# Performance work log

Measured on AMD Instinct MI355X. Metric: run time of the kernel, lower is better.

The kernel has to match this reference:

```python
import jax, jax.numpy as jnp
import numpy as np

N = 50000      # nodes
E = 625000     # edges
D_IN = 128     # in_feats
D_OUT = 128    # out_feats


def setup_inputs() -> dict:
    key = jax.random.key(0)
    k1, k2, k3, k4, k5, k6 = jax.random.split(key, 6)
    feat = jax.random.normal(k1, (N, D_IN), dtype=jnp.float32)
    affine = jax.random.uniform(k2, (E,), dtype=jnp.float32)
    src = jax.random.randint(k3, (E,), 0, N, dtype=jnp.int32)
    dst = jnp.sort(jax.random.randint(k4, (E,), 0, N, dtype=jnp.int32))
    # Linear(in_feats*2, out_feats): torch stores weight [out, in]; use [in, out] here
    bound = 1.0 / np.sqrt(2 * D_IN)
    W = jax.random.uniform(k5, (2 * D_IN, D_OUT), minval=-bound, maxval=bound, dtype=jnp.float32)
    b = jax.random.uniform(k6, (D_OUT,), minval=-bound, maxval=bound, dtype=jnp.float32)
    return {"feat": feat, "affine": affine, "src": src, "dst": dst, "W": W, "b": b}


def reference(feat, affine, src, dst, W, b):
    # u_mul_e: per-edge message = srcfeat[src] * edge scalar 'affine'
    msg = feat[src] * affine[:, None]                      # [E, D_IN]
    # fn.sum: scatter-add messages to destination nodes
    agg = jax.ops.segment_sum(msg, dst, num_segments=N)    # [N, D_IN]
    # concat dst features with aggregated neighborhood, then linear
    gcn_feat = jnp.concatenate([feat, agg], axis=-1)       # [N, 2*D_IN]
    return gcn_feat @ W + b                                # [N, D_OUT]
```

## Files before the change

### kernel.cpp

```cpp
#include <hip/hip_runtime.h>

#define N_NODES 50000
#define E_EDGES 625000
#define D 128

typedef __attribute__((ext_vector_type(8)))  short  short8;
typedef __attribute__((ext_vector_type(16))) float  floatx16;

static __device__ inline unsigned short f2bf(float f) {
    union { float f; unsigned u; } v; v.f = f;
    unsigned r = v.u + 0x7FFFu + ((v.u >> 16) & 1u);
    return (unsigned short)(r >> 16);
}
static __device__ inline float bflo(unsigned p) { return __uint_as_float(p << 16); }
static __device__ inline float bfhi(unsigned p) { return __uint_as_float(p & 0xFFFF0000u); }

__global__ __launch_bounds__(256) void prep_kernel(const int* __restrict__ dst,
                                                   const float* __restrict__ W,
                                                   const int* __restrict__ src,
                                                   const float* __restrict__ affine,
                                                   int* __restrict__ rowptr,
                                                   unsigned short* __restrict__ wimg,
                                                   uint2* __restrict__ meta) {
    int t = blockIdx.x * 256 + threadIdx.x;
    if (t < E_EDGES) {
        int d1 = dst[t];
        int d0 = (t == 0) ? -1 : dst[t - 1];
        for (int n = d0 + 1; n <= d1; ++n) rowptr[n] = t;
        if (t == E_EDGES - 1)
            for (int n = d1 + 1; n <= N_NODES; ++n) rowptr[n] = E_EDGES;
        uint2 m;
        m.x = (unsigned)src[t];
        m.y = __float_as_uint(affine[t]);
        meta[t] = m;
    }
    if (t < 4096) {
        int n = t & 127;
        int c = (t >> 7) & 15;
        int h = t >> 11;
        int krow = h * 128 + c * 8;
        short8 v;
        #pragma unroll
        for (int j = 0; j < 8; ++j)
            v[j] = (short)f2bf(W[(size_t)(krow + j) * D + n]);
        *((short8*)wimg + t) = v;
    }
}

#define NB_M 391

__global__ __launch_bounds__(256, 2) void gemm_mfma(const float* __restrict__ feat,
                                                    const unsigned short* __restrict__ wimg,
                                                    unsigned short* __restrict__ Z1b,
                                                    unsigned short* __restrict__ Y) {
    __shared__ short8 Bls[4096];

    int tid = threadIdx.x;
    int b   = blockIdx.x;

    const short8* wsrc = (const short8*)wimg;
    #pragma unroll
    for (int i = 0; i < 16; ++i)
        Bls[tid + i * 256] = wsrc[tid + i * 256];

    int wave = tid >> 6;
    int lane = tid & 63;
    int m = lane & 31;
    int g = lane >> 5;
    int row0   = b * 128 + wave * 32;
    int row_a  = row0 + m;
    int rclamp = row_a < N_NODES ? row_a : 0;

    short8 fa[8];
    const float* ap = feat + (size_t)rclamp * D + g * 8;
    #pragma unroll
    for (int ks = 0; ks < 8; ++ks) {
        float4 u = *(const float4*)(ap + ks * 16);
        float4 v = *(const float4*)(ap + ks * 16 + 4);
        short8 a;
        a[0] = (short)f2bf(u.x); a[1] = (short)f2bf(u.y);
        a[2] = (short)f2bf(u.z); a[3] = (short)f2bf(u.w);
        a[4] = (short)f2bf(v.x); a[5] = (short)f2bf(v.y);
        a[6] = (short)f2bf(v.z); a[7] = (short)f2bf(v.w);
        fa[ks] = a;
    }
    __syncthreads();

    #pragma unroll
    for (int h = 0; h < 2; ++h) {
        unsigned short* dstbuf = h ? Y : Z1b;
        #pragma unroll
        for (int t4 = 0; t4 < 4; ++t4) {
            int n = t4 * 32 + m;
            floatx16 acc = {0,0,0,0, 0,0,0,0, 0,0,0,0, 0,0,0,0};
            #pragma unroll
            for (int ks = 0; ks < 8; ++ks) {
                short8 bb = Bls[h * 2048 + (ks * 2 + g) * 128 + n];
                acc = __builtin_amdgcn_mfma_f32_32x32x16_bf16(fa[ks], bb, acc, 0, 0, 0);
            }
            #pragma unroll
            for (int r = 0; r < 16; ++r) {
                int row = row0 + (r & 3) + 8 * (r >> 2) + 4 * g;
                if (row < N_NODES) dstbuf[(size_t)row * D + n] = f2bf(acc[r]);
            }
        }
    }
}

__global__ __launch_bounds__(256) void agg_add(const unsigned short* __restrict__ Y,
                                               const unsigned short* __restrict__ Z1b,
                                               const uint2* __restrict__ meta,
                                               const int* __restrict__ rowptr,
                                               const float* __restrict__ bias,
                                               float* __restrict__ out) {
    int wave = threadIdx.x >> 6;
    int lane = threadIdx.x & 63;
    int n = blockIdx.x * 4 + wave;
    if (n >= N_NODES) return;
    int lo = rowptr[n], hi = rowptr[n + 1];
    int g  = lane >> 4;
    int jj = (lane & 15) << 3;
    const unsigned short* Yj = Y + jj;

    uint4  z  = *(const uint4*)(Z1b + (size_t)n * D + jj);
    float4 b0 = *(const float4*)(bias + jj);
    float4 b1 = *(const float4*)(bias + jj + 4);

    float acc[8] = {0,0,0,0,0,0,0,0};

    for (int e0 = lo; e0 < hi; e0 += 16) {
        uint2 md[4];
        #pragma unroll
        for (int u = 0; u < 4; ++u) {
            int i = e0 + u * 4 + g;
            md[u] = meta[i < hi ? i : lo];
        }
        float w[4];
        uint4 p[4];
        #pragma unroll
        for (int u = 0; u < 4; ++u) {
            int i = e0 + u * 4 + g;
            w[u] = (i < hi) ? __uint_as_float(md[u].y) : 0.f;
            p[u] = *(const uint4*)(Yj + (size_t)md[u].x * D);
        }
        #pragma unroll
        for (int u = 0; u < 4; ++u) {
            acc[0] += bflo(p[u].x) * w[u];  acc[1] += bfhi(p[u].x) * w[u];
            acc[2] += bflo(p[u].y) * w[u];  acc[3] += bfhi(p[u].y) * w[u];
            acc[4] += bflo(p[u].z) * w[u];  acc[5] += bfhi(p[u].z) * w[u];
            acc[6] += bflo(p[u].w) * w[u];  acc[7] += bfhi(p[u].w) * w[u];
        }
    }

    #pragma unroll
    for (int r = 0; r < 8; ++r) {
        acc[r] += __shfl_xor(acc[r], 16);
        acc[r] += __shfl_xor(acc[r], 32);
    }

    if (g == 0) {
        float* op = out + (size_t)n * D + jj;
        float4 o0, o1;
        o0.x = bflo(z.x) + b0.x + acc[0];  o0.y = bfhi(z.x) + b0.y + acc[1];
        o0.z = bflo(z.y) + b0.z + acc[2];  o0.w = bfhi(z.y) + b0.w + acc[3];
        o1.x = bflo(z.z) + b1.x + acc[4];  o1.y = bfhi(z.z) + b1.y + acc[5];
        o1.z = bflo(z.w) + b1.z + acc[6];  o1.w = bfhi(z.w) + b1.w + acc[7];
        *(float4*)op       = o0;
        *(float4*)(op + 4) = o1;
    }
}

extern "C" void kernel_launch(void* const* d_in, const int* in_sizes, int n_in,
                              void* d_out, int out_size, void* d_ws, size_t ws_size,
                              hipStream_t stream) {
    const float* feat   = (const float*)d_in[0];
    const float* affine = (const float*)d_in[1];
    const int*   src    = (const int*)  d_in[2];
    const int*   dst    = (const int*)  d_in[3];
    const float* W      = (const float*)d_in[4];
    const float* bias   = (const float*)d_in[5];
    float*       out    = (float*)d_out;

    unsigned short* wimg   = (unsigned short*)d_ws;
    int*            rowptr = (int*)((char*)d_ws + 65536);
    uint2*          meta   = (uint2*)((char*)d_ws + 266240);
    unsigned short* Y      = (unsigned short*)((char*)d_ws + 5267456);
    unsigned short* Z1b    = (unsigned short*)((char*)d_ws + 18067456);

    prep_kernel<<<(E_EDGES + 255) / 256, 256, 0, stream>>>(dst, W, src, affine,
                                                           rowptr, wimg, meta);
    gemm_mfma<<<NB_M, 256, 0, stream>>>(feat, wimg, Z1b, Y);
    agg_add<<<(N_NODES + 3) / 4, 256, 0, stream>>>(Y, Z1b, meta, rowptr, bias, out);
    agg_add<<<(N_NODES + 3) / 4, 256, 0, stream>>>(Y, Z1b, meta, rowptr, bias, out);
}
```

Baseline: 152.1 us.

## Fuse edge prep into GEMM launch and drop duplicate aggregation launch

Merges the prep kernel and the MFMA GEMM into one launch. Extra blocks beyond the GEMM grid build rowptr and the packed edge metadata, while each GEMM block converts W to bf16 straight into shared memory instead of reading a prebuilt image. It also removes a second, redundant launch of the aggregation kernel, which recomputed and rewrote the same output. This saves launch overhead and a full extra gather pass. In exchange, every GEMM block now does strided fp32 reads of W and its own conversion.

```diff
diff --git a/kernel.cpp b/kernel.cpp
--- a/kernel.cpp
+++ b/kernel.cpp
@@ -3,6 +3,9 @@
 #define N_NODES 50000
 #define E_EDGES 625000
 #define D 128
+
+#define NB_M 391
+#define PREP_BLOCKS ((E_EDGES + 255) / 256)
 
 typedef __attribute__((ext_vector_type(8)))  short  short8;
 typedef __attribute__((ext_vector_type(16))) float  floatx16;
@@ -15,59 +18,56 @@
 static __device__ inline float bflo(unsigned p) { return __uint_as_float(p << 16); }
 static __device__ inline float bfhi(unsigned p) { return __uint_as_float(p & 0xFFFF0000u); }
 
-__global__ __launch_bounds__(256) void prep_kernel(const int* __restrict__ dst,
-                                                   const float* __restrict__ W,
-                                                   const int* __restrict__ src,
-                                                   const float* __restrict__ affine,
-                                                   int* __restrict__ rowptr,
-                                                   unsigned short* __restrict__ wimg,
-                                                   uint2* __restrict__ meta) {
-    int t = blockIdx.x * 256 + threadIdx.x;
-    if (t < E_EDGES) {
-        int d1 = dst[t];
-        int d0 = (t == 0) ? -1 : dst[t - 1];
-        for (int n = d0 + 1; n <= d1; ++n) rowptr[n] = t;
-        if (t == E_EDGES - 1)
-            for (int n = d1 + 1; n <= N_NODES; ++n) rowptr[n] = E_EDGES;
-        uint2 m;
-        m.x = (unsigned)src[t];
-        m.y = __float_as_uint(affine[t]);
-        meta[t] = m;
+__global__ __launch_bounds__(256, 2) void fused_prep_gemm(
+        const float* __restrict__ feat,
+        const float* __restrict__ W,
+        const int*   __restrict__ dst,
+        const int*   __restrict__ src,
+        const float* __restrict__ affine,
+        int*            __restrict__ rowptr,
+        uint2*          __restrict__ meta,
+        unsigned short* __restrict__ Z1b,
+        unsigned short* __restrict__ Y) {
+    __shared__ short8 Bls[4096];
+
+    int tid = threadIdx.x;
+    int bid = blockIdx.x;
+
+    if (bid >= NB_M) {
+        int t = (bid - NB_M) * 256 + tid;
+        if (t < E_EDGES) {
+            int d1 = dst[t];
+            int d0 = (t == 0) ? -1 : dst[t - 1];
+            for (int n = d0 + 1; n <= d1; ++n) rowptr[n] = t;
+            if (t == E_EDGES - 1)
+                for (int n = d1 + 1; n <= N_NODES; ++n) rowptr[n] = E_EDGES;
+            uint2 m;
+            m.x = (unsigned)src[t];
+            m.y = __float_as_uint(affine[t]);
+            meta[t] = m;
+        }
+        return;
     }
-    if (t < 4096) {
-        int n = t & 127;
-        int c = (t >> 7) & 15;
-        int h = t >> 11;
+
+    #pragma unroll
+    for (int i = 0; i < 16; ++i) {
+        int s = tid + i * 256;
+        int n = s & 127;
+        int c = (s >> 7) & 15;
+        int h = s >> 11;
         int krow = h * 128 + c * 8;
         short8 v;
         #pragma unroll
         for (int j = 0; j < 8; ++j)
             v[j] = (short)f2bf(W[(size_t)(krow + j) * D + n]);
-        *((short8*)wimg + t) = v;
+        Bls[s] = v;
     }
-}
-
-#define NB_M 391
-
-__global__ __launch_bounds__(256, 2) void gemm_mfma(const float* __restrict__ feat,
-                                                    const unsigned short* __restrict__ wimg,
-                                                    unsigned short* __restrict__ Z1b,
-                                                    unsigned short* __restrict__ Y) {
-    __shared__ short8 Bls[4096];
-
-    int tid = threadIdx.x;
-    int b   = blockIdx.x;
-
-    const short8* wsrc = (const short8*)wimg;
-    #pragma unroll
-    for (int i = 0; i < 16; ++i)
-        Bls[tid + i * 256] = wsrc[tid + i * 256];
 
     int wave = tid >> 6;
     int lane = tid & 63;
     int m = lane & 31;
     int g = lane >> 5;
-    int row0   = b * 128 + wave * 32;
+    int row0   = bid * 128 + wave * 32;
     int row_a  = row0 + m;
     int rclamp = row_a < N_NODES ? row_a : 0;
 
@@ -181,15 +181,12 @@
     const float* bias   = (const float*)d_in[5];
     float*       out    = (float*)d_out;
 
-    unsigned short* wimg   = (unsigned short*)d_ws;
     int*            rowptr = (int*)((char*)d_ws + 65536);
     uint2*          meta   = (uint2*)((char*)d_ws + 266240);
     unsigned short* Y      = (unsigned short*)((char*)d_ws + 5267456);
     unsigned short* Z1b    = (unsigned short*)((char*)d_ws + 18067456);
 
-    prep_kernel<<<(E_EDGES + 255) / 256, 256, 0, stream>>>(dst, W, src, affine,
-                                                           rowptr, wimg, meta);
-    gemm_mfma<<<NB_M, 256, 0, stream>>>(feat, wimg, Z1b, Y);
-    agg_add<<<(N_NODES + 3) / 4, 256, 0, stream>>>(Y, Z1b, meta, rowptr, bias, out);
+    fused_prep_gemm<<<NB_M + PREP_BLOCKS, 256, 0, stream>>>(
+        feat, W, dst, src, affine, rowptr, meta, Z1b, Y);
     agg_add<<<(N_NODES + 3) / 4, 256, 0, stream>>>(Y, Z1b, meta, rowptr, bias, out);
 }
```

Result: faster. 124.1 us (-18.4%).
